# Kernel optimization log

Measured on AMD Instinct MI355X. Metric: run time of the kernel, lower is better.

## Reference

```python
import jax, jax.numpy as jnp
import numpy as np

N_NODES = 50000
N_EDGES = 800000
N_FEAT = 128
N_GRAPHS = 512
OUT_DIM = 128


def gcn_conv(x, W, b, src, dst, ew, n):
    """PyG GCNConv: h = x @ W; add self-loops (weight 1); symmetric norm
    D^-1/2 A D^-1/2 with edge weights; scatter-add messages src->dst; + bias."""
    h = x @ W  # [n, out]
    loop = jnp.arange(n)
    s = jnp.concatenate([src, loop])
    d = jnp.concatenate([dst, loop])
    w = jnp.concatenate([ew, jnp.ones((n,), x.dtype)])
    deg = jax.ops.segment_sum(w, d, num_segments=n)
    dinv = jnp.where(deg > 0, jax.lax.rsqrt(deg), 0.0)
    norm = dinv[s] * w * dinv[d]  # [E+n]
    out = jax.ops.segment_sum(h[s] * norm[:, None], d, num_segments=n)
    return out + b


def setup_inputs() -> dict:
    key = jax.random.key(0)
    ks = jax.random.split(key, 12)
    F = N_FEAT
    x = jax.random.normal(ks[0], (N_NODES, F), jnp.float32)
    edge_index = jax.random.randint(ks[1], (2, N_EDGES), 0, N_NODES, jnp.int64)
    edge_attr = jax.random.uniform(ks[2], (N_EDGES,), jnp.float32)
    # deterministic sorted graph assignment -> no empty graphs (avoids -inf in max pool)
    batch = (jnp.arange(N_NODES, dtype=jnp.int64) * N_GRAPHS) // N_NODES
    def lin(k, fi, fo):
        s = 1.0 / np.sqrt(fi)
        return jax.random.uniform(k, (fi, fo), jnp.float32, -s, s)
    return {
        "x": x, "edge_attr": edge_attr,
        "W1": lin(ks[3], F, F), "b1": jnp.zeros((F,), jnp.float32),
        "W2": lin(ks[4], F, 2 * F), "b2": jnp.zeros((2 * F,), jnp.float32),
        "W3": lin(ks[5], 2 * F, 4 * F), "b3": jnp.zeros((4 * F,), jnp.float32),
        "Wf1": lin(ks[6], 4 * F, 1024), "bf1": jnp.zeros((1024,), jnp.float32),
        "Wf2": lin(ks[7], 1024, OUT_DIM), "bf2": jnp.zeros((OUT_DIM,), jnp.float32),
        "edge_index": edge_index, "batch": batch,
    }


def reference(x, edge_attr, W1, b1, W2, b2, W3, b3, Wf1, bf1, Wf2, bf2,
              edge_index, batch):
    n = x.shape[0]
    src, dst = edge_index[0], edge_index[1]
    h = jax.nn.relu(gcn_conv(x, W1, b1, src, dst, edge_attr, n))
    h = jax.nn.relu(gcn_conv(h, W2, b2, src, dst, edge_attr, n))
    h = jax.nn.relu(gcn_conv(h, W3, b3, src, dst, edge_attr, n))
    # global max pool over nodes per graph
    g = jax.ops.segment_max(h, batch, num_segments=N_GRAPHS)  # [G, 4F]
    g = jax.nn.relu(g @ Wf1 + bf1)
    # dropout is identity in eval mode
    out = g @ Wf2 + bf2
    return out
```

## Files before the change

### kernel.cpp

```cpp
#include <hip/hip_runtime.h>

#define NNODES 50000
#define NEDGES 800000
#define NGRAPH 512
#define DCAP 64

typedef short bf16x8 __attribute__((ext_vector_type(8)));
typedef unsigned short u16x8 __attribute__((ext_vector_type(8)));
typedef float f32x4 __attribute__((ext_vector_type(4)));
typedef unsigned long long u64;

static __device__ __forceinline__ float b2f(unsigned short u) {
    return __uint_as_float(((unsigned)u) << 16);
}
static __device__ __forceinline__ unsigned short f2b(float f) {
    unsigned u = __float_as_uint(f);
    unsigned r = (u + 0x7fffu + ((u >> 16) & 1u)) >> 16;
    return (unsigned short)r;
}

static __device__ __forceinline__ void ldrow(const unsigned short* X, size_t off, float (&v)[2]) {
    unsigned u = *(const unsigned*)(X + off);
    v[0] = b2f((unsigned short)(u & 0xffff));
    v[1] = b2f((unsigned short)(u >> 16));
}
static __device__ __forceinline__ void ldrow(const unsigned short* X, size_t off, float (&v)[4]) {
    uint2 u = *(const uint2*)(X + off);
    v[0] = b2f((unsigned short)(u.x & 0xffff));
    v[1] = b2f((unsigned short)(u.x >> 16));
    v[2] = b2f((unsigned short)(u.y & 0xffff));
    v[3] = b2f((unsigned short)(u.y >> 16));
}

__global__ void k_setup(u64* deg_cnt, int* gp) {
    int i = blockIdx.x * 256 + threadIdx.x;
    if (i < NNODES) deg_cnt[i] = (u64)(1u << 24);
    if (i < NGRAPH * 512) gp[i] = 0;
}

__global__ __launch_bounds__(256) void k_count(const int4* __restrict__ ei_s,
                                               const int4* __restrict__ ei_d,
                                               const float4* __restrict__ ew4,
                                               u64* deg_cnt,
                                               unsigned* __restrict__ edges) {
    int t = blockIdx.x * 256 + threadIdx.x;
    if (t >= NEDGES / 4) return;
    int4 ss = ei_s[t];
    int4 dd = ei_d[t];
    float4 ww = ew4[t];
    int s[4] = {ss.x, ss.y, ss.z, ss.w};
    int d[4] = {dd.x, dd.y, dd.z, dd.w};
    float w[4] = {ww.x, ww.y, ww.z, ww.w};
    int slot[4];
    #pragma unroll
    for (int u = 0; u < 4; ++u) {
        unsigned fixed = __float2uint_rn(w[u] * 16777216.0f);
        u64 old = atomicAdd(&deg_cnt[d[u]], ((u64)1 << 32) | fixed);
        slot[u] = (int)(old >> 32);
        if (slot[u] > DCAP - 1) slot[u] = DCAP - 1;
    }
    #pragma unroll
    for (int u = 0; u < 4; ++u)
        edges[((unsigned)d[u] << 6) | slot[u]] = ((unsigned)f2b(w[u]) << 16) | (unsigned)s[u];
}

__global__ void k_prep(const u64* __restrict__ deg_cnt, float* __restrict__ dinv) {
    int i = blockIdx.x * 256 + threadIdx.x;
    if (i < NNODES)
        dinv[i] = rsqrtf((float)(unsigned)(deg_cnt[i] & 0xffffffffull) * 5.9604645e-8f);
}

__global__ void k_wt_all(const float* __restrict__ W1, const float* __restrict__ W2,
                         const float* __restrict__ W3, const float* __restrict__ Wf1,
                         const float* __restrict__ Wf2,
                         unsigned short* __restrict__ T1, unsigned short* __restrict__ T2,
                         unsigned short* __restrict__ T3, unsigned short* __restrict__ Tf1,
                         unsigned short* __restrict__ Tf2) {
    int i = blockIdx.x * 256 + threadIdx.x;
    const float* W; unsigned short* T; int K, ns;
    if (i < 16384)        { W = W1;  T = T1;  K = 128;  ns = 7;  }
    else if (i < 49152)   { W = W2;  T = T2;  K = 128;  ns = 8;  i -= 16384; }
    else if (i < 180224)  { W = W3;  T = T3;  K = 256;  ns = 9;  i -= 49152; }
    else if (i < 704512)  { W = Wf1; T = Tf1; K = 512;  ns = 10; i -= 180224; }
    else if (i < 835584)  { W = Wf2; T = Tf2; K = 1024; ns = 7;  i -= 704512; }
    else return;
    int k = i >> ns, n = i & ((1 << ns) - 1);
    T[(size_t)n * K + k] = f2b(W[i]);
}

__global__ void k_cvt4(const float* __restrict__ X, const float* __restrict__ dinv,
                       unsigned short* __restrict__ Y, int n4) {
    int i = blockIdx.x * 256 + threadIdx.x;
    if (i < n4) {
        float4 v = ((const float4*)X)[i];
        float d = dinv[i >> 5];
        uint2 o;
        o.x = (unsigned)f2b(v.x * d) | ((unsigned)f2b(v.y * d) << 16);
        o.y = (unsigned)f2b(v.z * d) | ((unsigned)f2b(v.w * d) << 16);
        ((uint2*)Y)[i] = o;
    }
}

template <int VEC>
__global__ __launch_bounds__(256) void k_aggregate(const unsigned short* __restrict__ X,
                                                   const u64* __restrict__ deg_cnt,
                                                   const unsigned* __restrict__ edges,
                                                   const float* __restrict__ dinv,
                                                   unsigned short* __restrict__ Z) {
    const int F = 64 * VEC;
    const int wave = threadIdx.x >> 6, lane = threadIdx.x & 63;
    const int node = blockIdx.x * 4 + wave;
    if (node >= NNODES) return;
    const int fo = lane * VEC;
    const float di = dinv[node];
    const int cnt = (int)(deg_cnt[node] >> 32);
    const unsigned* erow = edges + ((unsigned)node << 6);

    float acc[VEC], v[VEC];
    ldrow(X, (size_t)node * F + fo, v);
    #pragma unroll
    for (int j = 0; j < VEC; ++j) acc[j] = v[j];

    int e = 0;
    for (; e + 8 <= cnt; e += 8) {
        unsigned pk[8];
        float vv[8][VEC];
        #pragma unroll
        for (int u = 0; u < 8; ++u) pk[u] = erow[e + u];
        #pragma unroll
        for (int u = 0; u < 8; ++u) ldrow(X, (size_t)(pk[u] & 0xffffu) * F + fo, vv[u]);
        #pragma unroll
        for (int u = 0; u < 8; ++u) {
            float c = b2f((unsigned short)(pk[u] >> 16));
            #pragma unroll
            for (int j = 0; j < VEC; ++j) acc[j] += c * vv[u][j];
        }
    }
    for (; e + 4 <= cnt; e += 4) {
        unsigned pk[4];
        float vv[4][VEC];
        #pragma unroll
        for (int u = 0; u < 4; ++u) pk[u] = erow[e + u];
        #pragma unroll
        for (int u = 0; u < 4; ++u) ldrow(X, (size_t)(pk[u] & 0xffffu) * F + fo, vv[u]);
        #pragma unroll
        for (int u = 0; u < 4; ++u) {
            float c = b2f((unsigned short)(pk[u] >> 16));
            #pragma unroll
            for (int j = 0; j < VEC; ++j) acc[j] += c * vv[u][j];
        }
    }
    for (; e < cnt; ++e) {
        unsigned pe = erow[e];
        float c = b2f((unsigned short)(pe >> 16));
        ldrow(X, (size_t)(pe & 0xffffu) * F + fo, v);
        #pragma unroll
        for (int j = 0; j < VEC; ++j) acc[j] += c * v[j];
    }

    if constexpr (VEC == 2) {
        unsigned o = (unsigned)f2b(di * acc[0]) | ((unsigned)f2b(di * acc[1]) << 16);
        *(unsigned*)(Z + (size_t)node * F + fo) = o;
    } else {
        uint2 o;
        o.x = (unsigned)f2b(di * acc[0]) | ((unsigned)f2b(di * acc[1]) << 16);
        o.y = (unsigned)f2b(di * acc[2]) | ((unsigned)f2b(di * acc[3]) << 16);
        *(uint2*)(Z + (size_t)node * F + fo) = o;
    }
}

template <int CMODE, int AFP>
__global__ __launch_bounds__(256) void k_gemm_mfma(const void* __restrict__ Av,
                                                   const unsigned short* __restrict__ WT,
                                                   const float* __restrict__ bias,
                                                   void* __restrict__ Cv,
                                                   const int* __restrict__ batch,
                                                   int* __restrict__ gp,
                                                   const float* __restrict__ rscale,
                                                   int M, int N, int K) {
    constexpr int LDK = 40;
    __shared__ unsigned short As[64 * LDK];
    __shared__ unsigned short Bs[128 * LDK];
    const int tid = threadIdx.x;
    const int m0 = blockIdx.y * 64, n0 = blockIdx.x * 128;
    const int wave = tid >> 6, lane = tid & 63;
    const int wm = (wave >> 1) * 32;
    const int wn = (wave & 1) * 64;
    const int quad = lane >> 4, mrow = lane & 15;

    const int ar = tid >> 2;
    const int ak = (tid & 3) * 8;
    const bool arow_ok = (m0 + ar) < M;
    const size_t aoff = (size_t)(m0 + ar) * K + ak;
    const unsigned short* Bg0 = WT + (size_t)(n0 + ar) * K + ak;
    const unsigned short* Bg1 = WT + (size_t)(n0 + ar + 64) * K + ak;

    f32x4 acc[2][4] = {};

    for (int k0 = 0; k0 < K; k0 += 32) {
        u16x8 av = {};
        if (arow_ok) {
            if constexpr (AFP) {
                const float* Af = (const float*)Av + aoff + k0;
                float4 f0 = *(const float4*)Af;
                float4 f1 = *(const float4*)(Af + 4);
                av[0] = (short)f2b(f0.x); av[1] = (short)f2b(f0.y);
                av[2] = (short)f2b(f0.z); av[3] = (short)f2b(f0.w);
                av[4] = (short)f2b(f1.x); av[5] = (short)f2b(f1.y);
                av[6] = (short)f2b(f1.z); av[7] = (short)f2b(f1.w);
            } else {
                av = *(const u16x8*)((const unsigned short*)Av + aoff + k0);
            }
        }
        u16x8 bv0 = *(const u16x8*)(Bg0 + k0);
        u16x8 bv1 = *(const u16x8*)(Bg1 + k0);
        *(u16x8*)&As[ar * LDK + ak] = av;
        *(u16x8*)&Bs[ar * LDK + ak] = bv0;
        *(u16x8*)&Bs[(ar + 64) * LDK + ak] = bv1;
        __syncthreads();
        bf16x8 af[2], bf[4];
        #pragma unroll
        for (int mt = 0; mt < 2; ++mt)
            af[mt] = *(const bf16x8*)&As[(wm + mt * 16 + mrow) * LDK + quad * 8];
        #pragma unroll
        for (int nt = 0; nt < 4; ++nt)
            bf[nt] = *(const bf16x8*)&Bs[(wn + nt * 16 + mrow) * LDK + quad * 8];
        #pragma unroll
        for (int mt = 0; mt < 2; ++mt)
            #pragma unroll
            for (int nt = 0; nt < 4; ++nt)
                acc[mt][nt] = __builtin_amdgcn_mfma_f32_16x16x32_bf16(af[mt], bf[nt], acc[mt][nt], 0, 0, 0);
        __syncthreads();
    }

    float bn[4];
    #pragma unroll
    for (int nt = 0; nt < 4; ++nt) bn[nt] = bias[n0 + wn + nt * 16 + mrow];

    if constexpr (CMODE == 0) {
        unsigned short* C = (unsigned short*)Cv;
        #pragma unroll
        for (int mt = 0; mt < 2; ++mt) {
            #pragma unroll
            for (int r = 0; r < 4; ++r) {
                int row = m0 + wm + mt * 16 + quad * 4 + r;
                if (row < M) {
                    float rs = rscale ? rscale[row] : 1.0f;
                    #pragma unroll
                    for (int nt = 0; nt < 4; ++nt) {
                        float v = fmaxf(acc[mt][nt][r] + bn[nt], 0.f) * rs;
                        C[(size_t)row * N + n0 + wn + nt * 16 + mrow] = f2b(v);
                    }
                }
            }
        }
    } else if constexpr (CMODE == 1) {
        float* C = (float*)Cv;
        #pragma unroll
        for (int mt = 0; mt < 2; ++mt) {
            #pragma unroll
            for (int r = 0; r < 4; ++r) {
                int row = m0 + wm + mt * 16 + quad * 4 + r;
                if (row < M) {
                    #pragma unroll
                    for (int nt = 0; nt < 4; ++nt)
                        C[(size_t)row * N + n0 + wn + nt * 16 + mrow] = acc[mt][nt][r] + bn[nt];
                }
            }
        }
    } else {
        __shared__ float pools[2][2][128];
        const int g0 = batch[m0];
        int last = m0 + 63; if (last >= M) last = M - 1;
        const int gl = batch[last];
        int  gid[8];
        bool rok[8];
        #pragma unroll
        for (int mt = 0; mt < 2; ++mt)
            #pragma unroll
            for (int r = 0; r < 4; ++r) {
                int row = m0 + wm + mt * 16 + quad * 4 + r;
                rok[mt * 4 + r] = row < M;
                gid[mt * 4 + r] = (row < M) ? batch[row] : -1;
            }
        #pragma unroll
        for (int nt = 0; nt < 4; ++nt) {
            float v0 = 0.f, v1 = 0.f;
            #pragma unroll
            for (int mt = 0; mt < 2; ++mt)
                #pragma unroll
                for (int r = 0; r < 4; ++r) {
                    if (rok[mt * 4 + r]) {
                        float v = fmaxf(acc[mt][nt][r] + bn[nt], 0.f);
                        if (gid[mt * 4 + r] == g0) v0 = fmaxf(v0, v);
                        else v1 = fmaxf(v1, v);
                    }
                }
            v0 = fmaxf(v0, __shfl_xor(v0, 16, 64));
            v0 = fmaxf(v0, __shfl_xor(v0, 32, 64));
            v1 = fmaxf(v1, __shfl_xor(v1, 16, 64));
            v1 = fmaxf(v1, __shfl_xor(v1, 32, 64));
            if (quad == 0) {
                int c = wn + nt * 16 + mrow;
                pools[wm >> 5][0][c] = v0;
                pools[wm >> 5][1][c] = v1;
            }
        }
        __syncthreads();
        int c = tid & 127, gi = tid >> 7;
        float v = fmaxf(pools[0][gi][c], pools[1][gi][c]);
        int g = gi ? gl : g0;
        if (gi == 0 || gl != g0)
            atomicMax(&gp[(size_t)g * N + n0 + c], __float_as_int(v));
    }
}

extern "C" void kernel_launch(void* const* d_in, const int* in_sizes, int n_in,
                              void* d_out, int out_size, void* d_ws, size_t ws_size,
                              hipStream_t stream) {
    const float* x   = (const float*)d_in[0];
    const float* ew  = (const float*)d_in[1];
    const float* W1  = (const float*)d_in[2];
    const float* b1  = (const float*)d_in[3];
    const float* W2  = (const float*)d_in[4];
    const float* b2  = (const float*)d_in[5];
    const float* W3  = (const float*)d_in[6];
    const float* b3  = (const float*)d_in[7];
    const float* Wf1 = (const float*)d_in[8];
    const float* bf1 = (const float*)d_in[9];
    const float* Wf2 = (const float*)d_in[10];
    const float* bf2 = (const float*)d_in[11];
    const int* ei    = (const int*)d_in[12];
    const int* batch = (const int*)d_in[13];
    float* out = (float*)d_out;
    (void)in_sizes; (void)n_in; (void)out_size; (void)ws_size;

    char* p = (char*)d_ws;
    auto alloc = [&](size_t bytes) -> char* {
        char* r = p;
        p += (bytes + 255) & ~(size_t)255;
        return r;
    };
    const int nbN = (NNODES + 255) / 256;
    u64*   deg_cnt = (u64*)alloc((size_t)NNODES * 8);
    float* dinv   = (float*)alloc((size_t)NNODES * 4);
    unsigned* edges = (unsigned*)alloc((size_t)NNODES * DCAP * 4);
    int*   gp     = (int*)  alloc((size_t)NGRAPH * 512 * 4);
    unsigned short* f1   = (unsigned short*)alloc((size_t)NGRAPH * 1024 * 2);
    unsigned short* wt1  = (unsigned short*)alloc((size_t)128 * 128 * 2);
    unsigned short* wt2  = (unsigned short*)alloc((size_t)256 * 128 * 2);
    unsigned short* wt3  = (unsigned short*)alloc((size_t)512 * 256 * 2);
    unsigned short* wtf1 = (unsigned short*)alloc((size_t)1024 * 512 * 2);
    unsigned short* wtf2 = (unsigned short*)alloc((size_t)128 * 1024 * 2);
    unsigned short* bufA = (unsigned short*)alloc((size_t)NNODES * 256 * 2);
    unsigned short* bufB = (unsigned short*)alloc((size_t)NNODES * 256 * 2);
    unsigned short* x16  = bufB;

    const int MB = (NNODES + 63) / 64;
    const int AGG = (NNODES + 3) / 4;

    k_setup<<<1024, 256, 0, stream>>>(deg_cnt, gp);
    k_count<<<(NEDGES / 4 + 255) / 256, 256, 0, stream>>>(
        (const int4*)ei, (const int4*)(ei + NEDGES), (const float4*)ew, deg_cnt, edges);
    k_prep<<<nbN, 256, 0, stream>>>(deg_cnt, dinv);
    k_wt_all<<<(835584 + 255) / 256, 256, 0, stream>>>(W1, W2, W3, Wf1, Wf2,
                                                       wt1, wt2, wt3, wtf1, wtf2);
    k_cvt4<<<(NNODES * 32 + 255) / 256, 256, 0, stream>>>(x, dinv, x16, NNODES * 32);

    k_aggregate<2><<<AGG, 256, 0, stream>>>(x16, deg_cnt, edges, dinv, bufA);
    k_gemm_mfma<0, 0><<<dim3(1, MB), 256, 0, stream>>>(bufA, wt1, b1, bufB, batch, nullptr, dinv, NNODES, 128, 128);
    k_aggregate<2><<<AGG, 256, 0, stream>>>(bufB, deg_cnt, edges, dinv, bufA);
    k_gemm_mfma<0, 0><<<dim3(2, MB), 256, 0, stream>>>(bufA, wt2, b2, bufB, batch, nullptr, dinv, NNODES, 256, 128);
    k_aggregate<4><<<AGG, 256, 0, stream>>>(bufB, deg_cnt, edges, dinv, bufA);
    k_gemm_mfma<2, 0><<<dim3(4, MB), 256, 0, stream>>>(bufA, wt3, b3, nullptr, batch, gp, nullptr, NNODES, 512, 256);

    k_gemm_mfma<0, 1><<<dim3(8, NGRAPH / 64), 256, 0, stream>>>(gp, wtf1, bf1, f1, batch, nullptr, nullptr, NGRAPH, 1024, 512);
    k_gemm_mfma<1, 0><<<dim3(1, NGRAPH / 64), 256, 0, stream>>>(f1, wtf2, bf2, out, batch, nullptr, nullptr, NGRAPH, 128, 1024);
}
```

Measured before the change: 371.4 us.

## Stage GEMM A tile once in LDS and loop over all N columns; shrink DCAP

Adds a k_gemm_conv kernel for the three GCN layer GEMMs. Each block loads its full 64-row A tile, across the whole K, into shared memory once, then loops over every 128-column output tile, so A is no longer re-read once per column block. The max-pool epilogue moves into this kernel with an extra barrier per column tile. Separately, the per-node edge slot capacity drops from 64 to 48, shrinking the edge table, at the cost of a multiply instead of a shift for row addressing and a tighter bound on the maximum degree before edges are truncated. Grids shrink to one block per row tile, which lowers parallelism for the wider layers.

```diff
diff --git a/kernel.cpp b/kernel.cpp
--- a/kernel.cpp
+++ b/kernel.cpp
@@ -3,7 +3,7 @@
 #define NNODES 50000
 #define NEDGES 800000
 #define NGRAPH 512
-#define DCAP 64
+#define DCAP 48
 
 typedef short bf16x8 __attribute__((ext_vector_type(8)));
 typedef unsigned short u16x8 __attribute__((ext_vector_type(8)));
@@ -61,7 +61,7 @@
     }
     #pragma unroll
     for (int u = 0; u < 4; ++u)
-        edges[((unsigned)d[u] << 6) | slot[u]] = ((unsigned)f2b(w[u]) << 16) | (unsigned)s[u];
+        edges[(unsigned)d[u] * DCAP + slot[u]] = ((unsigned)f2b(w[u]) << 16) | (unsigned)s[u];
 }
 
 __global__ void k_prep(const u64* __restrict__ deg_cnt, float* __restrict__ dinv) {
@@ -114,7 +114,7 @@
     const int fo = lane * VEC;
     const float di = dinv[node];
     const int cnt = (int)(deg_cnt[node] >> 32);
-    const unsigned* erow = edges + ((unsigned)node << 6);
+    const unsigned* erow = edges + (unsigned)node * DCAP;
 
     float acc[VEC], v[VEC];
     ldrow(X, (size_t)node * F + fo, v);
@@ -169,14 +169,139 @@
     }
 }
 
+template <int CMODE, int KK>
+__global__ __launch_bounds__(256) void k_gemm_conv(const unsigned short* __restrict__ A,
+                                                   const unsigned short* __restrict__ WT,
+                                                   const float* __restrict__ bias,
+                                                   unsigned short* __restrict__ C,
+                                                   const int* __restrict__ batch,
+                                                   int* __restrict__ gp,
+                                                   const float* __restrict__ rscale,
+                                                   int M, int N) {
+    constexpr int LDA = KK + 8;
+    __shared__ unsigned short As[64 * LDA];
+    __shared__ unsigned short Bs[128 * 40];
+    __shared__ float pools[2][2][128];
+    const int tid = threadIdx.x;
+    const int m0 = blockIdx.x * 64;
+    const int wave = tid >> 6, lane = tid & 63;
+    const int wm = (wave >> 1) * 32;
+    const int wn = (wave & 1) * 64;
+    const int quad = lane >> 4, mrow = lane & 15;
+
+    #pragma unroll
+    for (int j = 0; j < KK / 32; ++j) {
+        int idx = j * 256 + tid;
+        int row = idx / (KK / 8);
+        int ko = (idx % (KK / 8)) * 8;
+        u16x8 av = {};
+        if (m0 + row < M) av = *(const u16x8*)(A + (size_t)(m0 + row) * KK + ko);
+        *(u16x8*)&As[row * LDA + ko] = av;
+    }
+    __syncthreads();
+
+    int g0 = 0, gl = 0;
+    int gid[8]; bool rok[8];
+    if constexpr (CMODE == 2) {
+        g0 = batch[m0];
+        int last = m0 + 63; if (last >= M) last = M - 1;
+        gl = batch[last];
+        #pragma unroll
+        for (int mt = 0; mt < 2; ++mt)
+            #pragma unroll
+            for (int r = 0; r < 4; ++r) {
+                int row = m0 + wm + mt * 16 + quad * 4 + r;
+                rok[mt * 4 + r] = row < M;
+                gid[mt * 4 + r] = (row < M) ? batch[row] : -1;
+            }
+    }
+
+    for (int n0 = 0; n0 < N; n0 += 128) {
+        f32x4 acc[2][4] = {};
+        for (int k0 = 0; k0 < KK; k0 += 32) {
+            #pragma unroll
+            for (int j = 0; j < 2; ++j) {
+                int idx = j * 256 + tid;
+                int row = idx >> 2;
+                int ko = (idx & 3) * 8;
+                *(u16x8*)&Bs[row * 40 + ko] = *(const u16x8*)(WT + (size_t)(n0 + row) * KK + k0 + ko);
+            }
+            __syncthreads();
+            bf16x8 af[2], bf[4];
+            #pragma unroll
+            for (int mt = 0; mt < 2; ++mt)
+                af[mt] = *(const bf16x8*)&As[(wm + mt * 16 + mrow) * LDA + k0 + quad * 8];
+            #pragma unroll
+            for (int nt = 0; nt < 4; ++nt)
+                bf[nt] = *(const bf16x8*)&Bs[(wn + nt * 16 + mrow) * 40 + quad * 8];
+            #pragma unroll
+            for (int mt = 0; mt < 2; ++mt)
+                #pragma unroll
+                for (int nt = 0; nt < 4; ++nt)
+                    acc[mt][nt] = __builtin_amdgcn_mfma_f32_16x16x32_bf16(af[mt], bf[nt], acc[mt][nt], 0, 0, 0);
+            __syncthreads();
+        }
+
+        float bn[4];
+        #pragma unroll
+        for (int nt = 0; nt < 4; ++nt) bn[nt] = bias[n0 + wn + nt * 16 + mrow];
+
+        if constexpr (CMODE == 0) {
+            #pragma unroll
+            for (int mt = 0; mt < 2; ++mt) {
+                #pragma unroll
+                for (int r = 0; r < 4; ++r) {
+                    int row = m0 + wm + mt * 16 + quad * 4 + r;
+                    if (row < M) {
+                        float rs = rscale ? rscale[row] : 1.0f;
+                        #pragma unroll
+                        for (int nt = 0; nt < 4; ++nt) {
+                            float v = fmaxf(acc[mt][nt][r] + bn[nt], 0.f) * rs;
+                            C[(size_t)row * N + n0 + wn + nt * 16 + mrow] = f2b(v);
+                        }
+                    }
+                }
+            }
+        } else {
+            #pragma unroll
+            for (int nt = 0; nt < 4; ++nt) {
+                float v0 = 0.f, v1 = 0.f;
+                #pragma unroll
+                for (int mt = 0; mt < 2; ++mt)
+                    #pragma unroll
+                    for (int r = 0; r < 4; ++r) {
+                        if (rok[mt * 4 + r]) {
+                            float v = fmaxf(acc[mt][nt][r] + bn[nt], 0.f);
+                            if (gid[mt * 4 + r] == g0) v0 = fmaxf(v0, v);
+                            else v1 = fmaxf(v1, v);
+                        }
+                    }
+                v0 = fmaxf(v0, __shfl_xor(v0, 16, 64));
+                v0 = fmaxf(v0, __shfl_xor(v0, 32, 64));
+                v1 = fmaxf(v1, __shfl_xor(v1, 16, 64));
+                v1 = fmaxf(v1, __shfl_xor(v1, 32, 64));
+                if (quad == 0) {
+                    int c = wn + nt * 16 + mrow;
+                    pools[wm >> 5][0][c] = v0;
+                    pools[wm >> 5][1][c] = v1;
+                }
+            }
+            __syncthreads();
+            int c = tid & 127, gi = tid >> 7;
+            float v = fmaxf(pools[0][gi][c], pools[1][gi][c]);
+            int g = gi ? gl : g0;
+            if (gi == 0 || gl != g0)
+                atomicMax(&gp[(size_t)g * N + n0 + c], __float_as_int(v));
+            __syncthreads();
+        }
+    }
+}
+
 template <int CMODE, int AFP>
 __global__ __launch_bounds__(256) void k_gemm_mfma(const void* __restrict__ Av,
                                                    const unsigned short* __restrict__ WT,
                                                    const float* __restrict__ bias,
                                                    void* __restrict__ Cv,
-                                                   const int* __restrict__ batch,
-                                                   int* __restrict__ gp,
-                                                   const float* __restrict__ rscale,
                                                    int M, int N, int K) {
     constexpr int LDK = 40;
     __shared__ unsigned short As[64 * LDK];
@@ -245,16 +370,15 @@
             for (int r = 0; r < 4; ++r) {
                 int row = m0 + wm + mt * 16 + quad * 4 + r;
                 if (row < M) {
-                    float rs = rscale ? rscale[row] : 1.0f;
                     #pragma unroll
                     for (int nt = 0; nt < 4; ++nt) {
-                        float v = fmaxf(acc[mt][nt][r] + bn[nt], 0.f) * rs;
+                        float v = fmaxf(acc[mt][nt][r] + bn[nt], 0.f);
                         C[(size_t)row * N + n0 + wn + nt * 16 + mrow] = f2b(v);
                     }
                 }
             }
         }
-    } else if constexpr (CMODE == 1) {
+    } else {
         float* C = (float*)Cv;
         #pragma unroll
         for (int mt = 0; mt < 2; ++mt) {
@@ -268,50 +392,6 @@
                 }
             }
         }
-    } else {
-        __shared__ float pools[2][2][128];
-        const int g0 = batch[m0];
-        int last = m0 + 63; if (last >= M) last = M - 1;
-        const int gl = batch[last];
-        int  gid[8];
-        bool rok[8];
-        #pragma unroll
-        for (int mt = 0; mt < 2; ++mt)
-            #pragma unroll
-            for (int r = 0; r < 4; ++r) {
-                int row = m0 + wm + mt * 16 + quad * 4 + r;
-                rok[mt * 4 + r] = row < M;
-                gid[mt * 4 + r] = (row < M) ? batch[row] : -1;
-            }
-        #pragma unroll
-        for (int nt = 0; nt < 4; ++nt) {
-            float v0 = 0.f, v1 = 0.f;
-            #pragma unroll
-            for (int mt = 0; mt < 2; ++mt)
-                #pragma unroll
-                for (int r = 0; r < 4; ++r) {
-                    if (rok[mt * 4 + r]) {
-                        float v = fmaxf(acc[mt][nt][r] + bn[nt], 0.f);
-                        if (gid[mt * 4 + r] == g0) v0 = fmaxf(v0, v);
-                        else v1 = fmaxf(v1, v);
-                    }
-                }
-            v0 = fmaxf(v0, __shfl_xor(v0, 16, 64));
-            v0 = fmaxf(v0, __shfl_xor(v0, 32, 64));
-            v1 = fmaxf(v1, __shfl_xor(v1, 16, 64));
-            v1 = fmaxf(v1, __shfl_xor(v1, 32, 64));
-            if (quad == 0) {
-                int c = wn + nt * 16 + mrow;
-                pools[wm >> 5][0][c] = v0;
-                pools[wm >> 5][1][c] = v1;
-            }
-        }
-        __syncthreads();
-        int c = tid & 127, gi = tid >> 7;
-        float v = fmaxf(pools[0][gi][c], pools[1][gi][c]);
-        int g = gi ? gl : g0;
-        if (gi == 0 || gl != g0)
-            atomicMax(&gp[(size_t)g * N + n0 + c], __float_as_int(v));
     }
 }
 
@@ -368,12 +448,12 @@
     k_cvt4<<<(NNODES * 32 + 255) / 256, 256, 0, stream>>>(x, dinv, x16, NNODES * 32);
 
     k_aggregate<2><<<AGG, 256, 0, stream>>>(x16, deg_cnt, edges, dinv, bufA);
-    k_gemm_mfma<0, 0><<<dim3(1, MB), 256, 0, stream>>>(bufA, wt1, b1, bufB, batch, nullptr, dinv, NNODES, 128, 128);
+    k_gemm_conv<0, 128><<<MB, 256, 0, stream>>>(bufA, wt1, b1, bufB, batch, nullptr, dinv, NNODES, 128);
     k_aggregate<2><<<AGG, 256, 0, stream>>>(bufB, deg_cnt, edges, dinv, bufA);
-    k_gemm_mfma<0, 0><<<dim3(2, MB), 256, 0, stream>>>(bufA, wt2, b2, bufB, batch, nullptr, dinv, NNODES, 256, 128);
+    k_gemm_conv<0, 128><<<MB, 256, 0, stream>>>(bufA, wt2, b2, bufB, batch, nullptr, dinv, NNODES, 256);
     k_aggregate<4><<<AGG, 256, 0, stream>>>(bufB, deg_cnt, edges, dinv, bufA);
-    k_gemm_mfma<2, 0><<<dim3(4, MB), 256, 0, stream>>>(bufA, wt3, b3, nullptr, batch, gp, nullptr, NNODES, 512, 256);
-
-    k_gemm_mfma<0, 1><<<dim3(8, NGRAPH / 64), 256, 0, stream>>>(gp, wtf1, bf1, f1, batch, nullptr, nullptr, NGRAPH, 1024, 512);
-    k_gemm_mfma<1, 0><<<dim3(1, NGRAPH / 64), 256, 0, stream>>>(f1, wtf2, bf2, out, batch, nullptr, nullptr, NGRAPH, 128, 1024);
-}
+    k_gemm_conv<2, 256><<<MB, 256, 0, stream>>>(bufA, wt3, b3, nullptr, batch, gp, nullptr, NNODES, 512);
+
+    k_gemm_mfma<0, 1><<<dim3(8, NGRAPH / 64), 256, 0, stream>>>(gp, wtf1, bf1, f1, NGRAPH, 1024, 512);
+    k_gemm_mfma<1, 0><<<dim3(1, NGRAPH / 64), 256, 0, stream>>>(f1, wtf2, bf2, out, NGRAPH, 128, 1024);
+}
```

Measured after the change: 387.4 us. +4.3%, slower.
